# Kernel tuning notes

Measured on AMD Instinct MI355X. Metric: run time of the kernel, lower is better.

Reference implementation:

```python
import jax, jax.numpy as jnp
import numpy as np

NUM_HEADS = 16
HEAD_DIM = 128
D_MODEL = 2048
SEQ = 2048
BATCH = 1


def setup_inputs() -> dict:
    key = jax.random.key(0)
    ks = jax.random.split(key, 7)
    s = 0.02
    return {
        "x": jax.random.normal(ks[0], (BATCH, SEQ, D_MODEL), dtype=jnp.float32),
        "q_w": jax.random.normal(ks[1], (D_MODEL, D_MODEL), dtype=jnp.float32) * s,
        "k_w": jax.random.normal(ks[2], (D_MODEL, D_MODEL), dtype=jnp.float32) * s,
        "v_w": jax.random.normal(ks[3], (D_MODEL, D_MODEL), dtype=jnp.float32) * s,
        "o_w": jax.random.normal(ks[4], (D_MODEL, D_MODEL), dtype=jnp.float32) * s,
        "gate_w": jax.random.normal(ks[5], (HEAD_DIM, HEAD_DIM), dtype=jnp.float32) * s,
        "gate_b": jax.random.normal(ks[6], (HEAD_DIM,), dtype=jnp.float32) * s,
    }


def reference(x, q_w, k_w, v_w, o_w, gate_w, gate_b):
    B, S, D = x.shape
    H, Hd = NUM_HEADS, HEAD_DIM
    # QKV projections (nn.Linear: y = x @ W^T), split into heads -> [B,H,S,Hd]
    def proj(w):
        return jnp.einsum('bsd,ed->bse', x, w).reshape(B, S, H, Hd).transpose(0, 2, 1, 3)
    q = proj(q_w)
    k = proj(k_w)
    v = proj(v_w)
    scale = 1.0 / jnp.sqrt(jnp.asarray(Hd, dtype=x.dtype))
    scores = jnp.einsum('bhqd,bhkd->bhqk', q, k) * scale  # [B,H,S,S]
    # causal mask
    causal = jnp.tril(jnp.ones((S, S), dtype=bool))
    scores = jnp.where(causal, scores, jnp.asarray(-1e30, dtype=scores.dtype))
    attn = jax.nn.softmax(scores, axis=-1)
    av = jnp.einsum('bhqk,bhkd->bhqd', attn, v)  # [B,H,S,Hd]
    # learned sigmoid gate computed from q, applied elementwise to attention output
    gate = jax.nn.sigmoid(jnp.einsum('bhqd,ed->bhqe', q, gate_w) + gate_b)
    out = av * gate
    out = out.transpose(0, 2, 1, 3).reshape(B, S, D)
    return jnp.einsum('bsd,ed->bse', out, o_w)
```

## Files before the change

kernel.cpp:

```cpp
#include <hip/hip_runtime.h>
#include <stdint.h>
#include <math.h>

#define DM 2048
#define NH 16
#define HD 128
#define LDQ (3 * DM)

typedef __bf16 bf16;
typedef __attribute__((ext_vector_type(8))) __bf16 bf16x8;
typedef __attribute__((ext_vector_type(4))) float f32x4;
typedef __attribute__((ext_vector_type(2))) unsigned int u32x2;

__device__ __forceinline__ void gload_lds16(const void* g, void* l) {
  __builtin_amdgcn_global_load_lds(
      (const __attribute__((address_space(1))) void*)g,
      (__attribute__((address_space(3))) void*)l,
      16, 0, 0);
}

__device__ __forceinline__ unsigned lds_addr(const void* p) {
  return (unsigned)(size_t)(const __attribute__((address_space(3))) void*)p;
}

template <int OFF>
__device__ __forceinline__ u32x2 tr_read(unsigned va) {
  u32x2 r;
  asm volatile("ds_read_b64_tr_b16 %0, %1 offset:%2"
               : "=v"(r) : "v"(va), "i"(OFF));
  return r;
}

#define TR4(dst, vd)                                        \
  dst[0] = tr_read<0>(vd);   dst[1] = tr_read<512>(vd);     \
  dst[2] = tr_read<1024>(vd); dst[3] = tr_read<1536>(vd);

__global__ __launch_bounds__(256) void cvt6(const float* xs, const float* qws,
                                            const float* kws, const float* vws,
                                            const float* ows, const float* gws,
                                            ushort* xd, ushort* w3d, ushort* owd,
                                            ushort* gwd) {
  const int y = blockIdx.y;
  const float4* s; ushort4* d; int n = (DM * DM) / 4;
  switch (y) {
    case 0: s = (const float4*)xs;  d = (ushort4*)xd;  break;
    case 1: s = (const float4*)qws; d = (ushort4*)w3d; break;
    case 2: s = (const float4*)kws; d = (ushort4*)(w3d + (size_t)DM * DM); break;
    case 3: s = (const float4*)vws; d = (ushort4*)(w3d + (size_t)2 * DM * DM); break;
    case 4: s = (const float4*)ows; d = (ushort4*)owd; break;
    default: s = (const float4*)gws; d = (ushort4*)gwd; n = (HD * HD) / 4; break;
  }
  int i = blockIdx.x * 256 + threadIdx.x;
  if (i >= n) return;
  float4 v = s[i];
  union { bf16 b[4]; ushort4 u; } r;
  r.b[0] = (bf16)v.x; r.b[1] = (bf16)v.y; r.b[2] = (bf16)v.z; r.b[3] = (bf16)v.w;
  d[i] = r.u;
}

template <typename OutT>
__global__ __launch_bounds__(256) void gemm128(const bf16* __restrict__ A,
                                               const bf16* __restrict__ Bw,
                                               OutT* __restrict__ C, int ldc) {
  __shared__ __align__(16) bf16 As[128 * 32];
  __shared__ __align__(16) bf16 Bs[128 * 32];
  const int tid = threadIdx.x;
  const int w = tid >> 6, l = tid & 63;
  const int wr = w >> 1, wc = w & 1;
  const int bx = blockIdx.x, by = blockIdx.y;
  const int lrow = l >> 2, lcol = (l & 3) * 8;
  const int fr = l & 15, fg = l >> 4;
  const bf16* Ag = A + (size_t)(by * 128 + w * 32 + lrow) * DM + lcol;
  const bf16* Bg = Bw + (size_t)(bx * 128 + w * 32 + lrow) * DM + lcol;
  bf16* Asw = &As[(w * 32) * 32];
  bf16* Bsw = &Bs[(w * 32) * 32];
  f32x4 acc[4][4] = {};
  for (int kt = 0; kt < DM / 32; ++kt) {
    const int ko = kt * 32;
    gload_lds16(Ag + ko, Asw);
    gload_lds16(Ag + ko + 16 * DM, Asw + 16 * 32);
    gload_lds16(Bg + ko, Bsw);
    gload_lds16(Bg + ko + 16 * DM, Bsw + 16 * 32);
    __syncthreads();
    bf16x8 af[4], bfr[4];
#pragma unroll
    for (int m = 0; m < 4; m++)
      af[m] = *(const bf16x8*)&As[(wr * 64 + m * 16 + fr) * 32 + fg * 8];
#pragma unroll
    for (int n = 0; n < 4; n++)
      bfr[n] = *(const bf16x8*)&Bs[(wc * 64 + n * 16 + fr) * 32 + fg * 8];
#pragma unroll
    for (int m = 0; m < 4; m++)
#pragma unroll
      for (int n = 0; n < 4; n++)
        acc[m][n] = __builtin_amdgcn_mfma_f32_16x16x32_bf16(af[m], bfr[n], acc[m][n], 0, 0, 0);
    __syncthreads();
  }
#pragma unroll
  for (int m = 0; m < 4; m++) {
    const int row0 = by * 128 + wr * 64 + m * 16 + fg * 4;
#pragma unroll
    for (int n = 0; n < 4; n++) {
      const int col = bx * 128 + wc * 64 + n * 16 + fr;
#pragma unroll
      for (int j = 0; j < 4; j++) C[(size_t)(row0 + j) * ldc + col] = (OutT)acc[m][n][j];
    }
  }
}

__global__ __launch_bounds__(256, 2) void attn_k(const bf16* __restrict__ QKV,
                                                 const bf16* __restrict__ GWb,
                                                 const float* __restrict__ gbias,
                                                 bf16* __restrict__ Gout) {
  __shared__ __align__(16) bf16 Ks[2][8192];
  __shared__ __align__(16) bf16 Vs[2][8192];
  const int gid = blockIdx.x;
  const int h = gid & 15;
  const int idx = gid >> 4;
  const int qt = (idx < 16) ? (31 - idx) : (idx - 16);
  const int tid = threadIdx.x;
  const int w = tid >> 6, l = tid & 63;
  const int fr = l & 15, fg = l >> 4;
  const int fg4 = fg * 4;
  const int qbase = qt * 64 + w * 16;
  const int qg = qbase + fr;
  const int qcol = h * HD;
  const int kcol = DM + h * HD;
  const int vcol = 2 * DM + h * HD;
  const float scale = 0.08838834764831845f;

  bf16x8 bq[4];
#pragma unroll
  for (int kt = 0; kt < 4; kt++)
    bq[kt] = *(const bf16x8*)&QKV[(size_t)(qbase + fr) * LDQ + qcol + kt * 32 + fg * 8];

  const bf16* vbase = QKV + (size_t)(l >> 1) * LDQ + vcol + (l & 1) * 8;
  bf16* Ksl = &Ks[0][0];
  bf16* Vsl = &Vs[0][0];
  const unsigned ldsb = lds_addr(Vsl) + 8u * (unsigned)l;

#define STAGE(buf, kvbase)                                                    \
  {                                                                           \
    _Pragma("unroll")                                                         \
    for (int c = 0; c < 4; c++) {                                             \
      const int i = w * 4 + c;                                                \
      const int krow = i * 4 + (l >> 4);                                      \
      const int c16 = (l & 15) ^ (krow & 7);                                  \
      gload_lds16(QKV + (size_t)((kvbase) + krow) * LDQ + kcol + c16 * 8,     \
                  Ksl + (buf) * 8192 + i * 512);                              \
      const int db = i >> 1, k0 = (i & 1) * 32;                               \
      gload_lds16(vbase + (size_t)((kvbase) + k0) * LDQ + db * 16,            \
                  Vsl + (buf) * 8192 + db * 1024 + k0 * 16);                  \
    }                                                                         \
  }

  f32x4 oacc[8] = {};
  float m = -1e30f, lsum = 0.f;

  STAGE(0, 0);
  __syncthreads();

  for (int t = 0; t <= qt; ++t) {
    const int kv0 = t * 64;
    const int cur = t & 1;
    bf16x8 ak[4][4];
    {
      const char* Kb = (const char*)(Ksl + cur * 8192);
      const int swz = fr & 7;
#pragma unroll
      for (int kb = 0; kb < 4; kb++) {
        const char* rp = Kb + (kb * 16 + fr) * 256;
#pragma unroll
        for (int kt = 0; kt < 4; kt++)
          ak[kb][kt] = *(const bf16x8*)(rp + (((kt * 4 + fg) ^ swz) << 4));
      }
    }
    if (t < qt) STAGE(cur ^ 1, kv0 + 64);
    f32x4 sacc[4] = {};
#pragma unroll
    for (int kb = 0; kb < 4; kb++)
#pragma unroll
      for (int kt = 0; kt < 4; kt++)
        sacc[kb] = __builtin_amdgcn_mfma_f32_16x16x32_bf16(ak[kb][kt], bq[kt], sacc[kb], 0, 0, 0);
    const bool diag = (t == qt);
    float p[4][4];
    float tmax = -1e30f;
#pragma unroll
    for (int kb = 0; kb < 4; kb++)
#pragma unroll
      for (int j = 0; j < 4; j++) {
        float s = sacc[kb][j] * scale;
        if (diag && (kv0 + kb * 16 + fg4 + j) > qg) s = -1e30f;
        p[kb][j] = s;
        tmax = fmaxf(tmax, s);
      }
    tmax = fmaxf(tmax, __shfl_xor(tmax, 16, 64));
    tmax = fmaxf(tmax, __shfl_xor(tmax, 32, 64));
    const float mnew = fmaxf(m, tmax);
    const float alpha = __expf(m - mnew);
    m = mnew;
    float sum = 0.f;
#pragma unroll
    for (int kb = 0; kb < 4; kb++)
#pragma unroll
      for (int j = 0; j < 4; j++) {
        const float e = __expf(p[kb][j] - m);
        p[kb][j] = e;
        sum += e;
      }
    sum += __shfl_xor(sum, 16, 64);
    sum += __shfl_xor(sum, 32, 64);
    lsum = lsum * alpha + sum;
    float alpha4[4];
#pragma unroll
    for (int j = 0; j < 4; j++) alpha4[j] = __shfl(alpha, fg4 + j, 64);
#pragma unroll
    for (int db = 0; db < 8; db++)
#pragma unroll
      for (int j = 0; j < 4; j++) oacc[db][j] *= alpha4[j];
    bf16x8 pa[2];
#pragma unroll
    for (int kc = 0; kc < 2; kc++)
#pragma unroll
      for (int e = 0; e < 8; e++) pa[kc][e] = (bf16)p[2 * kc + (e >> 2)][e & 3];
    {
      const unsigned va = ldsb + (unsigned)cur * 16384u;
      u32x2 ta[4], tb[4];
      TR4(ta, va);
#pragma unroll
      for (int db = 0; db < 8; db++) {
        const u32x2* curp = (db & 1) ? tb : ta;
        u32x2* nxtp = (db & 1) ? ta : tb;
        if (db < 7) {
          const unsigned vd = va + (unsigned)(db + 1) * 2048u;
          TR4(nxtp, vd);
          asm volatile("s_waitcnt lgkmcnt(4)" ::: "memory");
        } else {
          asm volatile("s_waitcnt lgkmcnt(0)" ::: "memory");
        }
        __builtin_amdgcn_sched_barrier(0);
        union { u32x2 h[2]; bf16x8 v; } u0, u1;
        u0.h[0] = curp[0]; u0.h[1] = curp[1];
        u1.h[0] = curp[2]; u1.h[1] = curp[3];
        oacc[db] = __builtin_amdgcn_mfma_f32_16x16x32_bf16(pa[0], u0.v, oacc[db], 0, 0, 0);
        oacc[db] = __builtin_amdgcn_mfma_f32_16x16x32_bf16(pa[1], u1.v, oacc[db], 0, 0, 0);
      }
    }
    __syncthreads();
  }

  const float rinv = 1.0f / lsum;
  float rinv4[4];
#pragma unroll
  for (int j = 0; j < 4; j++) rinv4[j] = __shfl(rinv, fg4 + j, 64);
  f32x4 gacc[8] = {};
#pragma unroll
  for (int kt = 0; kt < 4; kt++)
#pragma unroll
    for (int eb = 0; eb < 8; eb++) {
      const bf16x8 bg = *(const bf16x8*)&GWb[(eb * 16 + fr) * HD + kt * 32 + fg * 8];
      gacc[eb] = __builtin_amdgcn_mfma_f32_16x16x32_bf16(bq[kt], bg, gacc[eb], 0, 0, 0);
    }
#pragma unroll
  for (int db = 0; db < 8; db++) {
    const int e = db * 16 + fr;
    const float bias = gbias[e];
    const int col = h * HD + e;
#pragma unroll
    for (int j = 0; j < 4; j++) {
      const float gate = 1.0f / (1.0f + __expf(-(gacc[db][j] + bias)));
      const float o = oacc[db][j] * rinv4[j] * gate;
      Gout[(size_t)(qbase + fg4 + j) * DM + col] = (bf16)o;
    }
  }
#undef STAGE
}

extern "C" void kernel_launch(void* const* d_in, const int* in_sizes, int n_in,
                              void* d_out, int out_size, void* d_ws, size_t ws_size,
                              hipStream_t stream) {
  const float* x  = (const float*)d_in[0];
  const float* qw = (const float*)d_in[1];
  const float* kw = (const float*)d_in[2];
  const float* vw = (const float*)d_in[3];
  const float* ow = (const float*)d_in[4];
  const float* gw = (const float*)d_in[5];
  const float* gb = (const float*)d_in[6];
  float* out = (float*)d_out;

  char* ws = (char*)d_ws;
  const size_t MB = 1024 * 1024;
  bf16* xb  = (bf16*)(ws + 0 * MB);
  bf16* w3b = (bf16*)(ws + 8 * MB);
  bf16* owb = (bf16*)(ws + 32 * MB);
  bf16* gwb = (bf16*)(ws + 40 * MB);
  bf16* QKV = (bf16*)(ws + 41 * MB);
  bf16* Gb  = (bf16*)(ws + 65 * MB);

  cvt6<<<dim3(4096, 6), 256, 0, stream>>>(x, qw, kw, vw, ow, gw,
                                          (ushort*)xb, (ushort*)w3b,
                                          (ushort*)owb, (ushort*)gwb);

  gemm128<bf16><<<dim3(48, 16), 256, 0, stream>>>(xb, w3b, QKV, LDQ);

  attn_k<<<512, 256, 0, stream>>>(QKV, gwb, gb, Gb);

  gemm128<float><<<dim3(16, 16), 256, 0, stream>>>(Gb, owb, out, DM);
}
```

Baseline: 176.9 us.

## Add 256x256-tile QKV GEMM with 4-stage async LDS pipeline

Adds a new 512-thread GEMM kernel that computes 256x256 output tiles for the fused QKV projection, replacing the 128x128 kernel. It uses direct global-to-LDS loads into a 4-buffer ring with two tiles prefetched ahead, XOR-swizzled LDS layout, and raised wave priority around the MFMA block. Larger tiles are meant to raise operand reuse and cut global traffic, and the deeper pipeline hides load latency. The cost is only 192 blocks (one per CU) with a high register footprint, which may leave some CUs idle and limit latency hiding.

```diff
diff --git a/kernel.cpp b/kernel.cpp
--- a/kernel.cpp
+++ b/kernel.cpp
@@ -56,6 +56,93 @@
   union { bf16 b[4]; ushort4 u; } r;
   r.b[0] = (bf16)v.x; r.b[1] = (bf16)v.y; r.b[2] = (bf16)v.z; r.b[3] = (bf16)v.w;
   d[i] = r.u;
+}
+
+__global__ __launch_bounds__(512, 1) void gemm256(const bf16* __restrict__ A,
+                                                  const bf16* __restrict__ Bw,
+                                                  bf16* __restrict__ C, int ldc) {
+  __shared__ __align__(16) bf16 LA[4][8192];
+  __shared__ __align__(16) bf16 LB[4][8192];
+  const int tid = threadIdx.x;
+  const int w = tid >> 6, l = tid & 63;
+  const int wm = w >> 2, wn = w & 3;
+  const int fr = l & 15, fg = l >> 4;
+  const int bm0 = blockIdx.y * 256, bn0 = blockIdx.x * 256;
+
+  const int sr0 = w * 16 + (l >> 2);
+  const int su = l & 3;
+  const bf16* pa[2];
+  const bf16* pb[2];
+#pragma unroll
+  for (int i = 0; i < 2; i++) {
+    const int r = sr0 + i * 128;
+    const int col = (su ^ (r & 3)) * 8;
+    pa[i] = A + (size_t)(bm0 + r) * DM + col;
+    pb[i] = Bw + (size_t)(bn0 + r) * DM + col;
+  }
+
+#define STG(buf, kt)                                                     \
+  {                                                                      \
+    _Pragma("unroll")                                                    \
+    for (int i = 0; i < 2; i++) {                                        \
+      gload_lds16(pa[i] + (kt) * 32, &LA[buf][(i * 128 + w * 16) * 32]); \
+      gload_lds16(pb[i] + (kt) * 32, &LB[buf][(i * 128 + w * 16) * 32]); \
+    }                                                                    \
+  }
+
+  f32x4 acc[8][4] = {};
+
+  STG(0, 0);
+  STG(1, 1);
+
+  const int swzb = (fg ^ (fr & 3)) << 4;
+  const int arow0 = wm * 128 + fr;
+  const int brow0 = wn * 64 + fr;
+
+  for (int t = 0; t < 64; ++t) {
+    const int cur = t & 3;
+    if (t < 62) {
+      STG((t + 2) & 3, t + 2);
+      asm volatile("s_waitcnt vmcnt(8)" ::: "memory");
+    } else if (t == 62) {
+      asm volatile("s_waitcnt vmcnt(4)" ::: "memory");
+    } else {
+      asm volatile("s_waitcnt vmcnt(0)" ::: "memory");
+    }
+    __builtin_amdgcn_s_barrier();
+    asm volatile("" ::: "memory");
+
+    const char* Ab = (const char*)&LA[cur][0];
+    const char* Bb = (const char*)&LB[cur][0];
+    bf16x8 af[8], bfr[4];
+#pragma unroll
+    for (int m = 0; m < 8; m++)
+      af[m] = *(const bf16x8*)(Ab + (arow0 + m * 16) * 64 + swzb);
+#pragma unroll
+    for (int n = 0; n < 4; n++)
+      bfr[n] = *(const bf16x8*)(Bb + (brow0 + n * 16) * 64 + swzb);
+
+    __builtin_amdgcn_s_setprio(1);
+#pragma unroll
+    for (int m = 0; m < 8; m++)
+#pragma unroll
+      for (int n = 0; n < 4; n++)
+        acc[m][n] = __builtin_amdgcn_mfma_f32_16x16x32_bf16(af[m], bfr[n], acc[m][n], 0, 0, 0);
+    __builtin_amdgcn_s_setprio(0);
+    asm volatile("" ::: "memory");
+  }
+
+#pragma unroll
+  for (int m = 0; m < 8; m++) {
+    const int row0 = bm0 + wm * 128 + m * 16 + fg * 4;
+#pragma unroll
+    for (int n = 0; n < 4; n++) {
+      const int col = bn0 + wn * 64 + n * 16 + fr;
+#pragma unroll
+      for (int j = 0; j < 4; j++) C[(size_t)(row0 + j) * ldc + col] = (bf16)acc[m][n][j];
+    }
+  }
+#undef STG
 }
 
 template <typename OutT>
@@ -301,7 +388,7 @@
                                           (ushort*)xb, (ushort*)w3b,
                                           (ushort*)owb, (ushort*)gwb);
 
-  gemm128<bf16><<<dim3(48, 16), 256, 0, stream>>>(xb, w3b, QKV, LDQ);
+  gemm256<<<dim3(24, 8), 512, 0, stream>>>(xb, w3b, QKV, LDQ);
 
   attn_k<<<512, 256, 0, stream>>>(QKV, gwb, gb, Gb);
 
```

Result: no change. 179.2 us (+1.3%).

## Add dedicated 256x192 double-buffered QKV GEMM kernel with XCD-aware tile mapping

Applied to the files above, without the earlier changes.

Replaces the generic 128x128 GEMM for the fused QKV projection with a new 512-thread kernel. It uses 256x192 tiles and a K-step of 64, with double-buffered LDS filled through direct global-to-LDS loads and an XOR swizzle. The loop interleaves LDS fragment reads with MFMA groups under sched_barrier and setprio, and assigns blocks to XCDs so that column tiles sharing a chiplet reuse the same weights. The aim is higher arithmetic intensity and overlap of loads with compute, at the cost of heavy LDS use (about 112KB) and one block per CU.

```diff
diff --git a/kernel.cpp b/kernel.cpp
--- a/kernel.cpp
+++ b/kernel.cpp
@@ -56,6 +56,130 @@
   union { bf16 b[4]; ushort4 u; } r;
   r.b[0] = (bf16)v.x; r.b[1] = (bf16)v.y; r.b[2] = (bf16)v.z; r.b[3] = (bf16)v.w;
   d[i] = r.u;
+}
+
+__global__ __launch_bounds__(512, 1) void gemm_qkv(const bf16* __restrict__ A,
+                                                   const bf16* __restrict__ Bw,
+                                                   bf16* __restrict__ C) {
+  __shared__ __align__(16) bf16 LA[2][256 * 64];
+  __shared__ __align__(16) bf16 LB[2][192 * 64];
+  const int tid = threadIdx.x;
+  const int w = tid >> 6, l = tid & 63;
+  const int wm = w >> 2, wn = w & 3;
+  const int fr = l & 15, fg = l >> 4;
+  const int bid = blockIdx.x;
+  const int xcd = bid & 7, idx = bid >> 3;
+  const int bm0 = (idx >> 2) * 256;
+  const int bn0 = ((xcd << 2) | (idx & 3)) * 192;
+
+  const int srow = l >> 3;
+  const int sunit = (l & 7) ^ srow;
+  const bf16* pa = A + (size_t)(bm0 + w * 32 + srow) * DM + sunit * 8;
+  const bf16* pb = Bw + (size_t)(bn0 + w * 24 + srow) * DM + sunit * 8;
+
+#define STG(buf, kt)                                                        \
+  {                                                                         \
+    _Pragma("unroll")                                                       \
+    for (int i = 0; i < 4; i++)                                             \
+      gload_lds16(pa + (size_t)i * 8 * DM + (kt) * 64,                      \
+                  &LA[buf][(w * 32 + i * 8) * 64]);                         \
+    _Pragma("unroll")                                                       \
+    for (int i = 0; i < 3; i++)                                             \
+      gload_lds16(pb + (size_t)i * 8 * DM + (kt) * 64,                      \
+                  &LB[buf][(w * 24 + i * 8) * 64]);                         \
+  }
+
+  f32x4 acc[8][3] = {};
+
+  STG(0, 0);
+  STG(1, 1);
+  asm volatile("s_waitcnt vmcnt(7)" ::: "memory");
+  __builtin_amdgcn_s_barrier();
+
+  const int sw0 = ((fg) ^ (fr & 7)) << 4;
+  const int sw1 = ((4 + fg) ^ (fr & 7)) << 4;
+
+  for (int t = 0; t < 32; ++t) {
+    const int cur = t & 1;
+    const char* Ab = (const char*)&LA[cur][0];
+    const char* Bb = (const char*)&LB[cur][0];
+
+    bf16x8 aA[4], aB[4], bA[3], bB[3];
+#pragma unroll
+    for (int n = 0; n < 3; n++)
+      bA[n] = *(const bf16x8*)(Bb + (wn * 48 + n * 16 + fr) * 128 + sw0);
+#pragma unroll
+    for (int m = 0; m < 4; m++)
+      aA[m] = *(const bf16x8*)(Ab + (wm * 128 + m * 16 + fr) * 128 + sw0);
+#pragma unroll
+    for (int m = 0; m < 4; m++)
+      aB[m] = *(const bf16x8*)(Ab + (wm * 128 + (m + 4) * 16 + fr) * 128 + sw0);
+    __builtin_amdgcn_sched_barrier(0);
+    __builtin_amdgcn_s_setprio(1);
+#pragma unroll
+    for (int m = 0; m < 4; m++)
+#pragma unroll
+      for (int n = 0; n < 3; n++)
+        acc[m][n] = __builtin_amdgcn_mfma_f32_16x16x32_bf16(aA[m], bA[n], acc[m][n], 0, 0, 0);
+    __builtin_amdgcn_s_setprio(0);
+    __builtin_amdgcn_sched_barrier(0);
+#pragma unroll
+    for (int n = 0; n < 3; n++)
+      bB[n] = *(const bf16x8*)(Bb + (wn * 48 + n * 16 + fr) * 128 + sw1);
+#pragma unroll
+    for (int m = 0; m < 4; m++)
+      aA[m] = *(const bf16x8*)(Ab + (wm * 128 + m * 16 + fr) * 128 + sw1);
+    __builtin_amdgcn_sched_barrier(0);
+    __builtin_amdgcn_s_setprio(1);
+#pragma unroll
+    for (int m = 0; m < 4; m++)
+#pragma unroll
+      for (int n = 0; n < 3; n++)
+        acc[m + 4][n] = __builtin_amdgcn_mfma_f32_16x16x32_bf16(aB[m], bA[n], acc[m + 4][n], 0, 0, 0);
+    __builtin_amdgcn_s_setprio(0);
+    __builtin_amdgcn_sched_barrier(0);
+#pragma unroll
+    for (int m = 0; m < 4; m++)
+      aB[m] = *(const bf16x8*)(Ab + (wm * 128 + (m + 4) * 16 + fr) * 128 + sw1);
+    __builtin_amdgcn_sched_barrier(0);
+    __builtin_amdgcn_s_setprio(1);
+#pragma unroll
+    for (int m = 0; m < 4; m++)
+#pragma unroll
+      for (int n = 0; n < 3; n++)
+        acc[m][n] = __builtin_amdgcn_mfma_f32_16x16x32_bf16(aA[m], bB[n], acc[m][n], 0, 0, 0);
+    __builtin_amdgcn_s_setprio(0);
+    __builtin_amdgcn_sched_barrier(0);
+    __builtin_amdgcn_s_setprio(1);
+#pragma unroll
+    for (int m = 0; m < 4; m++)
+#pragma unroll
+      for (int n = 0; n < 3; n++)
+        acc[m + 4][n] = __builtin_amdgcn_mfma_f32_16x16x32_bf16(aB[m], bB[n], acc[m + 4][n], 0, 0, 0);
+    __builtin_amdgcn_s_setprio(0);
+    __builtin_amdgcn_sched_barrier(0);
+
+    __builtin_amdgcn_s_barrier();
+    if (t < 30) {
+      STG(cur, t + 2);
+      asm volatile("s_waitcnt vmcnt(7)" ::: "memory");
+    } else {
+      asm volatile("s_waitcnt vmcnt(0)" ::: "memory");
+    }
+    __builtin_amdgcn_s_barrier();
+  }
+
+#pragma unroll
+  for (int m = 0; m < 8; m++) {
+    const int row0 = bm0 + wm * 128 + m * 16 + fg * 4;
+#pragma unroll
+    for (int n = 0; n < 3; n++) {
+      const int col = bn0 + wn * 48 + n * 16 + fr;
+#pragma unroll
+      for (int j = 0; j < 4; j++) C[(size_t)(row0 + j) * LDQ + col] = (bf16)acc[m][n][j];
+    }
+  }
+#undef STG
 }
 
 template <typename OutT>
@@ -301,7 +425,7 @@
                                           (ushort*)xb, (ushort*)w3b,
                                           (ushort*)owb, (ushort*)gwb);
 
-  gemm128<bf16><<<dim3(48, 16), 256, 0, stream>>>(xb, w3b, QKV, LDQ);
+  gemm_qkv<<<256, 512, 0, stream>>>(xb, w3b, QKV);
 
   attn_k<<<512, 256, 0, stream>>>(QKV, gwb, gb, Gb);
 
```

Result: faster. 173.2 us (-2.1%).

## Replace QKV projection GEMM with 256x192-tile, 4-stage pipelined, XCD-aware kernel

Applied to the files above, without the earlier changes.

Adds a dedicated QKV projection GEMM that uses 512-thread blocks computing 256x192 output tiles. It streams K through a 4-stage LDS ring filled by direct global-to-LDS loads with XOR swizzling, and double-buffers register fragments. Block indices are remapped so that column tiles group by XCD. The goal is more reuse per loaded byte and better overlap of memory with MFMA than the 128x128 single-buffered GEMM. The cost is higher LDS and register use, and only 256 blocks, which is about one wave of blocks across the CUs.

```diff
diff --git a/kernel.cpp b/kernel.cpp
--- a/kernel.cpp
+++ b/kernel.cpp
@@ -56,6 +56,113 @@
   union { bf16 b[4]; ushort4 u; } r;
   r.b[0] = (bf16)v.x; r.b[1] = (bf16)v.y; r.b[2] = (bf16)v.z; r.b[3] = (bf16)v.w;
   d[i] = r.u;
+}
+
+__global__ __launch_bounds__(512, 2) void gemm_qkv(const bf16* __restrict__ A,
+                                                   const bf16* __restrict__ Bw,
+                                                   bf16* __restrict__ C) {
+  __shared__ __align__(16) bf16 LA[4 * 8192];
+  __shared__ __align__(16) bf16 LB[4 * 8192];
+  const int tid = threadIdx.x;
+  const int w = tid >> 6, l = tid & 63;
+  const int wm = w >> 2, wn = w & 3;
+  const int fr = l & 15, fg = l >> 4;
+  const int bid = blockIdx.x;
+  const int xcd = bid & 7, idx = bid >> 3;
+  const int bm0 = (idx >> 2) * 256;
+  const int bn0 = ((xcd << 2) | (idx & 3)) * 192;
+
+  const int lr = l >> 2;
+  const int su8 = ((l & 3) ^ (lr & 3)) * 8;
+  const int r0 = w * 32 + lr;
+  const int brc0 = (bn0 + r0 < bn0 + 192) ? r0 : (191);
+
+#define STAGE(hx)                                                              \
+  {                                                                            \
+    const int s_ = (hx) & 3;                                                   \
+    const size_t kc_ = (size_t)(hx) * 32;                                      \
+    _Pragma("unroll")                                                          \
+    for (int i = 0; i < 2; i++) {                                              \
+      const int ar = r0 + i * 16;                                              \
+      gload_lds16(A + (size_t)(bm0 + ar) * DM + kc_ + su8,                     \
+                  &LA[s_ * 8192 + (w * 32 + i * 16) * 32]);                    \
+      const int br = (ar < 192) ? ar : 191;                                    \
+      gload_lds16(Bw + (size_t)(bn0 + br) * DM + kc_ + su8,                    \
+                  &LB[s_ * 8192 + (w * 32 + i * 16) * 32]);                    \
+    }                                                                          \
+  }
+
+  const int rsw = (fg ^ (fr & 3)) << 4;
+  const int arb = (wm * 128 + fr) * 64;
+  const int brb = (wn * 48 + fr) * 64;
+
+#define READS(hx, RA, RB)                                                      \
+  {                                                                            \
+    const char* Ab_ = (const char*)&LA[((hx) & 3) * 8192];                     \
+    const char* Bb_ = (const char*)&LB[((hx) & 3) * 8192];                     \
+    _Pragma("unroll")                                                          \
+    for (int m = 0; m < 8; m++)                                                \
+      RA[m] = *(const bf16x8*)(Ab_ + arb + m * 1024 + rsw);                    \
+    _Pragma("unroll")                                                          \
+    for (int n = 0; n < 3; n++)                                                \
+      RB[n] = *(const bf16x8*)(Bb_ + brb + n * 1024 + rsw);                    \
+  }
+
+  f32x4 acc[8][3] = {};
+  bf16x8 aF0[8], bF0[3], aF1[8], bF1[3];
+
+  STAGE(0); STAGE(1); STAGE(2);
+  asm volatile("s_waitcnt vmcnt(4)" ::: "memory");
+  __builtin_amdgcn_s_barrier();
+  READS(0, aF0, bF0);
+
+#define BODY(h, CA, CB, NA, NB)                                                \
+  {                                                                            \
+    if ((h) + 3 < 64) STAGE((h) + 3);                                          \
+    if ((h) + 1 < 64) {                                                        \
+      READS((h) + 1, NA, NB);                                                  \
+      asm volatile("s_waitcnt lgkmcnt(11)" ::: "memory");                      \
+    } else {                                                                   \
+      asm volatile("s_waitcnt lgkmcnt(0)" ::: "memory");                       \
+    }                                                                          \
+    __builtin_amdgcn_sched_barrier(0);                                         \
+    __builtin_amdgcn_s_setprio(1);                                             \
+    _Pragma("unroll")                                                          \
+    for (int m = 0; m < 8; m++)                                                \
+      _Pragma("unroll")                                                        \
+      for (int n = 0; n < 3; n++)                                              \
+        acc[m][n] = __builtin_amdgcn_mfma_f32_16x16x32_bf16(CA[m], CB[n],      \
+                                                            acc[m][n], 0, 0, 0);\
+    __builtin_amdgcn_s_setprio(0);                                             \
+    __builtin_amdgcn_sched_barrier(0);                                         \
+    if ((h) < 63) {                                                            \
+      if ((h) <= 61) {                                                         \
+        asm volatile("s_waitcnt vmcnt(4)" ::: "memory");                       \
+      } else {                                                                 \
+        asm volatile("s_waitcnt vmcnt(0)" ::: "memory");                       \
+      }                                                                        \
+      __builtin_amdgcn_s_barrier();                                            \
+    }                                                                          \
+  }
+
+  for (int hh = 0; hh < 64; hh += 2) {
+    BODY(hh,     aF0, bF0, aF1, bF1);
+    BODY(hh + 1, aF1, bF1, aF0, bF0);
+  }
+
+#pragma unroll
+  for (int m = 0; m < 8; m++) {
+    const int row0 = bm0 + wm * 128 + m * 16 + fg * 4;
+#pragma unroll
+    for (int n = 0; n < 3; n++) {
+      const int col = bn0 + wn * 48 + n * 16 + fr;
+#pragma unroll
+      for (int j = 0; j < 4; j++) C[(size_t)(row0 + j) * LDQ + col] = (bf16)acc[m][n][j];
+    }
+  }
+#undef BODY
+#undef READS
+#undef STAGE
 }
 
 template <typename OutT>
@@ -239,9 +346,9 @@
           asm volatile("s_waitcnt lgkmcnt(0)" ::: "memory");
         }
         __builtin_amdgcn_sched_barrier(0);
-        union { u32x2 h[2]; bf16x8 v; } u0, u1;
-        u0.h[0] = curp[0]; u0.h[1] = curp[1];
-        u1.h[0] = curp[2]; u1.h[1] = curp[3];
+        union { u32x2 h2[2]; bf16x8 v; } u0, u1;
+        u0.h2[0] = curp[0]; u0.h2[1] = curp[1];
+        u1.h2[0] = curp[2]; u1.h2[1] = curp[3];
         oacc[db] = __builtin_amdgcn_mfma_f32_16x16x32_bf16(pa[0], u0.v, oacc[db], 0, 0, 0);
         oacc[db] = __builtin_amdgcn_mfma_f32_16x16x32_bf16(pa[1], u1.v, oacc[db], 0, 0, 0);
       }
@@ -301,7 +408,7 @@
                                           (ushort*)xb, (ushort*)w3b,
                                           (ushort*)owb, (ushort*)gwb);
 
-  gemm128<bf16><<<dim3(48, 16), 256, 0, stream>>>(xb, w3b, QKV, LDQ);
+  gemm_qkv<<<256, 512, 0, stream>>>(xb, w3b, QKV);
 
   attn_k<<<512, 256, 0, stream>>>(QKV, gwb, gb, Gb);
 
```

Result: slower. 190.9 us (+7.9%).
